# Optimization experiments

Measured on AMD Instinct MI355X. Metric: run time of the kernel, lower is better.

## Reference

```python
import jax, jax.numpy as jnp
import numpy as np

EPS = 1e-4
B, D, DOUT = 8192, 4096, 4096


def setup_inputs() -> dict:
    key = jax.random.key(0)
    k1, k2, k3 = jax.random.split(key, 3)
    x = jax.random.normal(k1, (B, D), dtype=jnp.float32)
    # Linear layer params (torch nn.Linear: y = x @ W.T + b)
    W = jax.random.normal(k2, (DOUT, D), dtype=jnp.float32) * (1.0 / np.sqrt(D))
    b = jax.random.normal(k3, (DOUT,), dtype=jnp.float32) * 0.01
    return {"x": x, "W": W, "b": b}


def reference(x, W, b):
    # hess = sum_b x[b] outer x[b] + eps*I  == X^T X + eps*I (a GEMM, not a
    # materialized [B,D,D] broadcast like the torch source)
    d = x.shape[1]
    hess = jnp.einsum('bi,bj->ij', x, x) + EPS * jnp.eye(d, dtype=x.dtype)
    out = x @ W.T + b  # wrapped nn.Linear
    return out, hess
```

## Files before the change

### kernel.cpp

```cpp
#include <hip/hip_runtime.h>
#include <hip/hip_bf16.h>

#define BDIM 8192
#define DDIM 4096
#define DOUTD 4096

typedef __attribute__((ext_vector_type(8))) short short8;
typedef __attribute__((ext_vector_type(16))) float floatx16;

__device__ inline unsigned short f32_to_bf16_rne(float f) {
    unsigned int u = __float_as_uint(f);
    unsigned int lsb = (u >> 16) & 1u;
    u += 0x7fffu + lsb;
    return (unsigned short)(u >> 16);
}

__device__ inline void gload_lds16(const void* g, void* lds) {
    __builtin_amdgcn_global_load_lds(
        (const __attribute__((address_space(1))) void*)g,
        (__attribute__((address_space(3))) void*)lds,
        16, 0, 0);
}

__global__ __launch_bounds__(256)
void convert_transpose_x(const float* __restrict__ x,
                         unsigned short* __restrict__ xb,
                         unsigned short* __restrict__ xT) {
    __shared__ __align__(16) unsigned short tile[64][72];
    const int t = threadIdx.x;
    const int tb = blockIdx.x * 64;
    const int td = blockIdx.y * 64;
#pragma unroll
    for (int p = 0; p < 4; ++p) {
        int c = t + p * 256;
        int row  = c >> 4;
        int col4 = (c & 15) << 2;
        float4 v = *(const float4*)&x[(size_t)(tb + row) * DDIM + td + col4];
        ushort4 o;
        o.x = f32_to_bf16_rne(v.x);
        o.y = f32_to_bf16_rne(v.y);
        o.z = f32_to_bf16_rne(v.z);
        o.w = f32_to_bf16_rne(v.w);
        *(ushort4*)&xb[(size_t)(tb + row) * DDIM + td + col4] = o;
        tile[col4 + 0][row] = o.x;
        tile[col4 + 1][row] = o.y;
        tile[col4 + 2][row] = o.z;
        tile[col4 + 3][row] = o.w;
    }
    __syncthreads();
#pragma unroll
    for (int p = 0; p < 4; ++p) {
        int c = t + p * 256;
        int drow = c >> 4;
        int b4   = (c & 15) << 2;
        ushort4 o = *(const ushort4*)&tile[drow][b4];
        *(ushort4*)&xT[(size_t)(td + drow) * BDIM + tb + b4] = o;
    }
}

__global__ __launch_bounds__(256)
void convert_w_kernel(const float* __restrict__ W, unsigned short* __restrict__ Wb) {
    size_t i = ((size_t)blockIdx.x * 256 + threadIdx.x) * 4;
    float4 v = *(const float4*)&W[i];
    ushort4 o;
    o.x = f32_to_bf16_rne(v.x);
    o.y = f32_to_bf16_rne(v.y);
    o.z = f32_to_bf16_rne(v.z);
    o.w = f32_to_bf16_rne(v.w);
    *(ushort4*)&Wb[i] = o;
}

#define CFENCE() asm volatile("" ::: "memory")
#define BAR() do { CFENCE(); __builtin_amdgcn_s_barrier(); CFENCE(); } while (0)
#define MFMA_BF16 __builtin_amdgcn_mfma_f32_32x32x16_bf16

template <bool HESS>
__global__ __launch_bounds__(512, 2)
void gemm256(const unsigned short* __restrict__ A,
             const unsigned short* __restrict__ B,
             const float* __restrict__ bias,
             float* __restrict__ C,
             int M, int N, int K) {
    __shared__ __align__(16) unsigned short As[32768];
    __shared__ __align__(16) unsigned short Bs[32768];

    const int t    = threadIdx.x;
    const int lane = t & 63;
    const int w    = t >> 6;
    const int lm   = lane & 31;
    const int hi   = lane >> 5;
    const int key  = lm >> 2;
    const int wm   = w >> 2;
    const int wn   = w & 3;
    const size_t bm = (size_t)blockIdx.y * 256;
    const size_t bn = (size_t)blockIdx.x * 256;
    const int NT = K >> 6;

    const int r8  = lane >> 3;
    const int c8  = lane & 7;
    const int rl0 = w * 16 + r8;
    const int rl1 = rl0 + 8;
    const int kc0 = c8 ^ ((w * 4 + (lane >> 5)) & 7);
    const int kc1 = c8 ^ ((w * 4 + 2 + (lane >> 5)) & 7);
    const unsigned short* gA0 = A + (bm + rl0) * (size_t)K + kc0 * 8;
    const unsigned short* gA1 = A + (bm + rl1) * (size_t)K + kc1 * 8;
    const unsigned short* gB0 = B + (bn + rl0) * (size_t)K + kc0 * 8;
    const unsigned short* gB1 = B + (bn + rl1) * (size_t)K + kc1 * 8;
    char* ldsA = (char*)As + w * 2048;
    char* ldsB = (char*)Bs + w * 2048;
    const size_t halfK = (size_t)128 * K;

#define STAGE_A(tj, h, buf) do {                                   \
        const size_t _ko = (size_t)(tj) * 64 + (size_t)(h) * halfK;\
        char* _d = ldsA + (buf) * 32768 + (h) * 16384;             \
        gload_lds16(gA0 + _ko, _d);                                \
        gload_lds16(gA1 + _ko, _d + 1024);                         \
    } while (0)
#define STAGE_B(tj, h, buf) do {                                   \
        const size_t _ko = (size_t)(tj) * 64 + (size_t)(h) * halfK;\
        char* _d = ldsB + (buf) * 32768 + (h) * 16384;             \
        gload_lds16(gB0 + _ko, _d);                                \
        gload_lds16(gB1 + _ko, _d + 1024);                         \
    } while (0)

    const int AROW = (wm * 128 + lm) * 64;
    const int BROW = (wn * 32 + lm) * 64;
    int swz[4];
#pragma unroll
    for (int s = 0; s < 4; ++s) swz[s] = (((2 * s + hi) ^ key) << 3);

    floatx16 acc[4][2];
#pragma unroll
    for (int i = 0; i < 4; ++i)
#pragma unroll
        for (int j = 0; j < 2; ++j)
#pragma unroll
            for (int g = 0; g < 16; ++g)
                acc[i][j][g] = 0.f;

    short8 af0[2][4], af1[2][4], bf[4];

    STAGE_B(0, 0, 0);
    STAGE_A(0, 0, 0);
    STAGE_A(0, 1, 0);
    STAGE_B(0, 1, 0);
    STAGE_B(1, 0, 1);
    STAGE_A(1, 0, 1);
    STAGE_A(1, 1, 1);
    asm volatile("s_waitcnt vmcnt(6)" ::: "memory");
    BAR();

    for (int j = 0; j < NT; ++j) {
        const int cur = j & 1;
        const int ab  = cur * 16384;

#pragma unroll
        for (int mi = 0; mi < 2; ++mi)
#pragma unroll
            for (int s = 0; s < 4; ++s)
                af0[mi][s] = *(const short8*)&As[ab + AROW + mi * 2048 + swz[s]];
#pragma unroll
        for (int s = 0; s < 4; ++s)
            bf[s] = *(const short8*)&Bs[ab + BROW + swz[s]];
        if (j + 1 < NT) STAGE_B(j + 1, 1, cur ^ 1);
        BAR();
        __builtin_amdgcn_s_setprio(1);
#pragma unroll
        for (int s = 0; s < 4; ++s) {
            acc[0][0] = MFMA_BF16(af0[0][s], bf[s], acc[0][0], 0, 0, 0);
            acc[1][0] = MFMA_BF16(af0[1][s], bf[s], acc[1][0], 0, 0, 0);
        }
        __builtin_amdgcn_s_setprio(0);
        asm volatile("s_waitcnt lgkmcnt(0)" ::: "memory");
        BAR();

#pragma unroll
        for (int mi = 0; mi < 2; ++mi)
#pragma unroll
            for (int s = 0; s < 4; ++s)
                af1[mi][s] = *(const short8*)&As[ab + AROW + 4096 + mi * 2048 + swz[s]];
        if (j + 2 < NT) STAGE_B(j + 2, 0, cur);
        BAR();
        __builtin_amdgcn_s_setprio(1);
#pragma unroll
        for (int s = 0; s < 4; ++s) {
            acc[2][0] = MFMA_BF16(af1[0][s], bf[s], acc[2][0], 0, 0, 0);
            acc[3][0] = MFMA_BF16(af1[1][s], bf[s], acc[3][0], 0, 0, 0);
        }
        __builtin_amdgcn_s_setprio(0);
        asm volatile("s_waitcnt lgkmcnt(0)" ::: "memory");
        BAR();

#pragma unroll
        for (int s = 0; s < 4; ++s)
            bf[s] = *(const short8*)&Bs[ab + BROW + 8192 + swz[s]];
        if (j + 2 < NT) STAGE_A(j + 2, 0, cur);
        BAR();
        __builtin_amdgcn_s_setprio(1);
#pragma unroll
        for (int s = 0; s < 4; ++s) {
            acc[2][1] = MFMA_BF16(af1[0][s], bf[s], acc[2][1], 0, 0, 0);
            acc[3][1] = MFMA_BF16(af1[1][s], bf[s], acc[3][1], 0, 0, 0);
        }
        __builtin_amdgcn_s_setprio(0);
        asm volatile("s_waitcnt lgkmcnt(0)" ::: "memory");
        BAR();

        if (j + 2 < NT) STAGE_A(j + 2, 1, cur);
        BAR();
        __builtin_amdgcn_s_setprio(1);
#pragma unroll
        for (int s = 0; s < 4; ++s) {
            acc[0][1] = MFMA_BF16(af0[0][s], bf[s], acc[0][1], 0, 0, 0);
            acc[1][1] = MFMA_BF16(af0[1][s], bf[s], acc[1][1], 0, 0, 0);
        }
        __builtin_amdgcn_s_setprio(0);
        if (j < NT - 2)       asm volatile("s_waitcnt vmcnt(6)" ::: "memory");
        else if (j == NT - 2) asm volatile("s_waitcnt vmcnt(0)" ::: "memory");
        BAR();
    }
#undef STAGE_A
#undef STAGE_B

    float bv[2];
#pragma unroll
    for (int n2 = 0; n2 < 2; ++n2)
        bv[n2] = HESS ? 0.f : bias[bn + n2 * 128 + wn * 32 + lm];
#pragma unroll
    for (int m4 = 0; m4 < 4; ++m4) {
        const size_t mbase = bm + wm * 128 + (m4 >> 1) * 64 + (m4 & 1) * 32 + 4 * hi;
#pragma unroll
        for (int n2 = 0; n2 < 2; ++n2) {
            const size_t n = bn + n2 * 128 + wn * 32 + lm;
#pragma unroll
            for (int reg = 0; reg < 16; ++reg) {
                const size_t m = mbase + (reg & 3) + 8 * (reg >> 2);
                float v = acc[m4][n2][reg] + bv[n2];
                if (HESS && m == n) v += 1e-4f;
                C[m * N + n] = v;
            }
        }
    }
}

extern "C" void kernel_launch(void* const* d_in, const int* in_sizes, int n_in,
                              void* d_out, int out_size, void* d_ws, size_t ws_size,
                              hipStream_t stream) {
    const float* x = (const float*)d_in[0];
    const float* W = (const float*)d_in[1];
    const float* b = (const float*)d_in[2];

    float* out  = (float*)d_out;
    float* hess = out + (size_t)BDIM * DOUTD;

    unsigned short* xb = (unsigned short*)d_ws;
    unsigned short* xT = xb + (size_t)BDIM * DDIM;
    unsigned short* Wb = xT + (size_t)BDIM * DDIM;

    convert_transpose_x<<<dim3(BDIM / 64, DDIM / 64), 256, 0, stream>>>(x, xb, xT);
    convert_w_kernel<<<((size_t)DOUTD * DDIM) / 1024, 256, 0, stream>>>(W, Wb);

    gemm256<false><<<dim3(DOUTD / 256, BDIM / 256), 512, 0, stream>>>(
        xb, Wb, b, out, BDIM, DOUTD, DDIM);
    gemm256<true><<<dim3(DDIM / 256, DDIM / 256), 512, 0, stream>>>(
        xT, xT, nullptr, hess, DDIM, DDIM, BDIM);
}
```

Before: 892.9 us.

## Split LDS tiles into two 32-wide K halves with 4-way XOR swizzle

Result: faster. 858.7 us (-3.8%).

```diff
diff --git a/kernel.cpp b/kernel.cpp
--- a/kernel.cpp
+++ b/kernel.cpp
@@ -89,45 +89,43 @@
     const int w    = t >> 6;
     const int lm   = lane & 31;
     const int hi   = lane >> 5;
-    const int key  = lm >> 2;
+    const int key2 = (lm >> 2) & 3;
     const int wm   = w >> 2;
     const int wn   = w & 3;
     const size_t bm = (size_t)blockIdx.y * 256;
     const size_t bn = (size_t)blockIdx.x * 256;
     const int NT = K >> 6;
 
-    const int r8  = lane >> 3;
-    const int c8  = lane & 7;
-    const int rl0 = w * 16 + r8;
-    const int rl1 = rl0 + 8;
-    const int kc0 = c8 ^ ((w * 4 + (lane >> 5)) & 7);
-    const int kc1 = c8 ^ ((w * 4 + 2 + (lane >> 5)) & 7);
-    const unsigned short* gA0 = A + (bm + rl0) * (size_t)K + kc0 * 8;
-    const unsigned short* gA1 = A + (bm + rl1) * (size_t)K + kc1 * 8;
-    const unsigned short* gB0 = B + (bn + rl0) * (size_t)K + kc0 * 8;
-    const unsigned short* gB1 = B + (bn + rl1) * (size_t)K + kc1 * 8;
-    char* ldsA = (char*)As + w * 2048;
-    char* ldsB = (char*)Bs + w * 2048;
-    const size_t halfK = (size_t)128 * K;
+    const int kh_w = w >> 2;
+    const int wq   = w & 3;
+    const int rsub = lane >> 2;
+    const int csrc = (lane & 3) ^ ((lane >> 4) & 3);
+    const unsigned short* gA0 = A + (bm + wq * 32 + rsub) * (size_t)K + kh_w * 32 + csrc * 8;
+    const unsigned short* gB0 = B + (bn + wq * 32 + rsub) * (size_t)K + kh_w * 32 + csrc * 8;
+    char* ldsA = (char*)As + kh_w * 16384 + wq * 2048;
+    char* ldsB = (char*)Bs + kh_w * 16384 + wq * 2048;
+    const size_t rowK16 = (size_t)16 * K;
+    const size_t halfK  = (size_t)128 * K;
 
 #define STAGE_A(tj, h, buf) do {                                   \
         const size_t _ko = (size_t)(tj) * 64 + (size_t)(h) * halfK;\
-        char* _d = ldsA + (buf) * 32768 + (h) * 16384;             \
+        char* _d = ldsA + (buf) * 32768 + (h) * 8192;              \
         gload_lds16(gA0 + _ko, _d);                                \
-        gload_lds16(gA1 + _ko, _d + 1024);                         \
+        gload_lds16(gA0 + _ko + rowK16, _d + 1024);                \
     } while (0)
 #define STAGE_B(tj, h, buf) do {                                   \
         const size_t _ko = (size_t)(tj) * 64 + (size_t)(h) * halfK;\
-        char* _d = ldsB + (buf) * 32768 + (h) * 16384;             \
+        char* _d = ldsB + (buf) * 32768 + (h) * 8192;              \
         gload_lds16(gB0 + _ko, _d);                                \
-        gload_lds16(gB1 + _ko, _d + 1024);                         \
+        gload_lds16(gB0 + _ko + rowK16, _d + 1024);                \
     } while (0)
 
-    const int AROW = (wm * 128 + lm) * 64;
-    const int BROW = (wn * 32 + lm) * 64;
-    int swz[4];
-#pragma unroll
-    for (int s = 0; s < 4; ++s) swz[s] = (((2 * s + hi) ^ key) << 3);
+    const int AROWb = (wm * 128 + lm) * 32;
+    const int BROWb = (wn * 32 + lm) * 32;
+    int pofs[4];
+#pragma unroll
+    for (int s = 0; s < 4; ++s)
+        pofs[s] = (s >> 1) * 8192 + ((((s & 1) * 2 + hi) ^ key2) * 8);
 
     floatx16 acc[4][2];
 #pragma unroll
@@ -158,10 +156,10 @@
         for (int mi = 0; mi < 2; ++mi)
 #pragma unroll
             for (int s = 0; s < 4; ++s)
-                af0[mi][s] = *(const short8*)&As[ab + AROW + mi * 2048 + swz[s]];
+                af0[mi][s] = *(const short8*)&As[ab + AROWb + mi * 1024 + pofs[s]];
 #pragma unroll
         for (int s = 0; s < 4; ++s)
-            bf[s] = *(const short8*)&Bs[ab + BROW + swz[s]];
+            bf[s] = *(const short8*)&Bs[ab + BROWb + pofs[s]];
         if (j + 1 < NT) STAGE_B(j + 1, 1, cur ^ 1);
         BAR();
         __builtin_amdgcn_s_setprio(1);
@@ -178,7 +176,7 @@
         for (int mi = 0; mi < 2; ++mi)
 #pragma unroll
             for (int s = 0; s < 4; ++s)
-                af1[mi][s] = *(const short8*)&As[ab + AROW + 4096 + mi * 2048 + swz[s]];
+                af1[mi][s] = *(const short8*)&As[ab + AROWb + 2048 + mi * 1024 + pofs[s]];
         if (j + 2 < NT) STAGE_B(j + 2, 0, cur);
         BAR();
         __builtin_amdgcn_s_setprio(1);
@@ -193,7 +191,7 @@
 
 #pragma unroll
         for (int s = 0; s < 4; ++s)
-            bf[s] = *(const short8*)&Bs[ab + BROW + 8192 + swz[s]];
+            bf[s] = *(const short8*)&Bs[ab + BROWb + 4096 + pofs[s]];
         if (j + 2 < NT) STAGE_A(j + 2, 0, cur);
         BAR();
         __builtin_amdgcn_s_setprio(1);
```
